# Kernel tuning notes

Measured on AMD Instinct MI355X. Metric: run time of the kernel, lower is better.

Reference implementation:

```python
import jax, jax.numpy as jnp
import numpy as np

DIM = 1024
NUM_HEADS = 16
HEAD_DIM = DIM // NUM_HEADS
SCALE = HEAD_DIM ** -0.5


def setup_inputs() -> dict:
    key = jax.random.key(0)
    k_x, k_qkv, k_proj, k_pb = jax.random.split(key, 4)
    B, N = 4, 2048
    x = jax.random.normal(k_x, (B, N, DIM), dtype=jnp.float32)
    # qkv: Linear(dim, 3*dim), qkv_bias=False -> no bias
    W_qkv = jax.random.normal(k_qkv, (DIM, 3 * DIM), dtype=jnp.float32) * (DIM ** -0.5)
    # proj: Linear(dim, dim) with bias (nn.Linear default)
    W_proj = jax.random.normal(k_proj, (DIM, DIM), dtype=jnp.float32) * (DIM ** -0.5)
    b_proj = jax.random.normal(k_pb, (DIM,), dtype=jnp.float32) * 0.01
    return {"x": x, "W_qkv": W_qkv, "W_proj": W_proj, "b_proj": b_proj}


def reference(x, W_qkv, W_proj, b_proj):
    B, N, C = x.shape
    H, D = NUM_HEADS, HEAD_DIM
    # qkv projection -> [B, N, 3, H, D] -> q,k,v each [B, H, N, D]
    qkv = (x @ W_qkv).reshape(B, N, 3, H, D)
    q, k, v = (jnp.moveaxis(qkv, 2, 0).transpose(0, 1, 3, 2, 4))  # [3,B,H,N,D]
    # attention scores [B, H, N, N], scaled QK^T (full matrix, as in source)
    attn = jnp.einsum('bhqd,bhkd->bhqk', q, k) * SCALE
    attn = jax.nn.softmax(attn, axis=-1)
    # attn @ V -> [B, H, N, D] -> [B, N, C]
    out = jnp.einsum('bhqk,bhkd->bhqd', attn, v)
    out = out.transpose(0, 2, 1, 3).reshape(B, N, C)
    # output projection
    return out @ W_proj + b_proj
```

## Files before the change

kernel.cpp:

```cpp
#include <hip/hip_runtime.h>
#include <hip/hip_bf16.h>

typedef __attribute__((ext_vector_type(8))) short short8;
typedef __attribute__((ext_vector_type(4))) short short4_t;
typedef __attribute__((ext_vector_type(4))) float floatx4;
typedef unsigned short u16;
typedef unsigned int u32;

#define SEQ 2048
#define NH 16
#define HD 64
#define CDIM 1024
#define MTOT 8192

__device__ __forceinline__ u16 f2bf(float f) {
  u32 u = __builtin_bit_cast(u32, f);
  u32 r = u + 0x7FFFu + ((u >> 16) & 1u);
  return (u16)(r >> 16);
}

__device__ __forceinline__ void gload16(const void* g, void* l) {
  __builtin_amdgcn_global_load_lds(
      (const __attribute__((address_space(1))) u32*)g,
      (__attribute__((address_space(3))) u32*)l, 16, 0, 0);
}

__global__ void cvt_x_kernel(const float* __restrict__ x, u16* __restrict__ xb) {
  size_t i = (size_t)blockIdx.x * 256 + threadIdx.x;
  const float4* xv = (const float4*)x;
  float4 a = xv[2 * i], c = xv[2 * i + 1];
  union { u16 h[8]; short8 v; } u;
  u.h[0] = f2bf(a.x); u.h[1] = f2bf(a.y); u.h[2] = f2bf(a.z); u.h[3] = f2bf(a.w);
  u.h[4] = f2bf(c.x); u.h[5] = f2bf(c.y); u.h[6] = f2bf(c.z); u.h[7] = f2bf(c.w);
  *(short8*)(xb + 8 * i) = u.v;
}

__global__ void transpose_w(const float* __restrict__ w, u16* __restrict__ wt,
                            int K, int N) {
  __shared__ float t[32][33];
  int n0 = blockIdx.x * 32, k0 = blockIdx.y * 32;
  int tr = threadIdx.x >> 5, tc = threadIdx.x & 31;
#pragma unroll
  for (int i = 0; i < 4; i++) {
    int r = tr + i * 8;
    t[r][tc] = w[(size_t)(k0 + r) * N + n0 + tc];
  }
  __syncthreads();
#pragma unroll
  for (int i = 0; i < 4; i++) {
    int r = tr + i * 8;
    wt[(size_t)(n0 + r) * K + k0 + tc] = f2bf(t[tc][r]);
  }
}

__global__ __launch_bounds__(256, 2) void gemm_qkv(
    const u16* __restrict__ A, const u16* __restrict__ BT,
    u16* __restrict__ qb, u16* __restrict__ kb, u16* __restrict__ vtb) {
  __shared__ u16 Ab[128 * 64];
  __shared__ u16 Bb[128 * 64];
  const int tid = threadIdx.x;
  const int w = tid >> 6, l = tid & 63;
  const int quad = l >> 4, l15 = l & 15;
  const int m0 = blockIdx.x * 128, n0 = blockIdx.y * 128;
  const int wr = w >> 1, wc = w & 1;

  floatx4 acc[4][4] = {};

  for (int k0 = 0; k0 < 1024; k0 += 64) {
    __syncthreads();
#pragma unroll
    for (int rnd = 0; rnd < 4; rnd++) {
      int ci = rnd * 256 + tid;
      int r = ci >> 3, pos = ci & 7;
      int c = pos ^ (r & 7);
      gload16(A + (size_t)(m0 + r) * 1024 + k0 + c * 8, (char*)Ab + ci * 16);
      gload16(BT + (size_t)(n0 + r) * 1024 + k0 + c * 8, (char*)Bb + ci * 16);
    }
    __syncthreads();
    short8 af[4][2], bf[4][2];
#pragma unroll
    for (int t = 0; t < 4; t++) {
      int ra = wr * 64 + t * 16 + l15;
      int ga = ra & 7;
#pragma unroll
      for (int ks = 0; ks < 2; ks++)
        af[t][ks] = *(short8*)((char*)Ab + ra * 128 + ((ks * 4 + quad) ^ ga) * 16);
      int rb = wc * 64 + t * 16 + l15;
      int gb = rb & 7;
#pragma unroll
      for (int ks = 0; ks < 2; ks++)
        bf[t][ks] = *(short8*)((char*)Bb + rb * 128 + ((ks * 4 + quad) ^ gb) * 16);
    }
#pragma unroll
    for (int ks = 0; ks < 2; ks++)
#pragma unroll
      for (int i = 0; i < 4; i++)
#pragma unroll
        for (int j = 0; j < 4; j++)
          acc[i][j] = __builtin_amdgcn_mfma_f32_16x16x32_bf16(af[i][ks], bf[j][ks], acc[i][j], 0, 0, 0);
  }

#pragma unroll
  for (int i = 0; i < 4; i++)
#pragma unroll
    for (int j = 0; j < 4; j++)
#pragma unroll
      for (int r = 0; r < 4; r++) {
        int m = m0 + wr * 64 + i * 16 + quad * 4 + r;
        int c = n0 + wc * 64 + j * 16 + l15;
        int b = m >> 11, n = m & 2047;
        int t = c >> 10, rem = c & 1023;
        int h = rem >> 6, d = rem & 63;
        int bh = b * NH + h;
        if (t == 0)      qb[((size_t)bh * SEQ + n) * HD + d] = f2bf(acc[i][j][r] * 0.18033688011112042f);
        else if (t == 1) kb[((size_t)bh * SEQ + n) * HD + d] = f2bf(acc[i][j][r]);
        else             vtb[((size_t)bh * HD + d) * SEQ + n] = f2bf(acc[i][j][r]);
      }
}

__global__ __launch_bounds__(256, 2) void gemm_proj(
    const u16* __restrict__ A, const u16* __restrict__ BT,
    const float* __restrict__ bias, float* __restrict__ out) {
  __shared__ u16 Ab[128 * 64];
  __shared__ u16 Bb[128 * 64];
  const int tid = threadIdx.x;
  const int w = tid >> 6, l = tid & 63;
  const int quad = l >> 4, l15 = l & 15;
  const int m0 = blockIdx.x * 128, n0 = blockIdx.y * 128;
  const int wr = w >> 1, wc = w & 1;

  floatx4 acc[4][4] = {};

  for (int k0 = 0; k0 < 1024; k0 += 64) {
    __syncthreads();
#pragma unroll
    for (int rnd = 0; rnd < 4; rnd++) {
      int ci = rnd * 256 + tid;
      int r = ci >> 3, pos = ci & 7;
      int c = pos ^ (r & 7);
      gload16(A + (size_t)(m0 + r) * 1024 + k0 + c * 8, (char*)Ab + ci * 16);
      gload16(BT + (size_t)(n0 + r) * 1024 + k0 + c * 8, (char*)Bb + ci * 16);
    }
    __syncthreads();
    short8 af[4][2], bf[4][2];
#pragma unroll
    for (int t = 0; t < 4; t++) {
      int ra = wr * 64 + t * 16 + l15;
      int ga = ra & 7;
#pragma unroll
      for (int ks = 0; ks < 2; ks++)
        af[t][ks] = *(short8*)((char*)Ab + ra * 128 + ((ks * 4 + quad) ^ ga) * 16);
      int rb = wc * 64 + t * 16 + l15;
      int gb = rb & 7;
#pragma unroll
      for (int ks = 0; ks < 2; ks++)
        bf[t][ks] = *(short8*)((char*)Bb + rb * 128 + ((ks * 4 + quad) ^ gb) * 16);
    }
#pragma unroll
    for (int ks = 0; ks < 2; ks++)
#pragma unroll
      for (int i = 0; i < 4; i++)
#pragma unroll
        for (int j = 0; j < 4; j++)
          acc[i][j] = __builtin_amdgcn_mfma_f32_16x16x32_bf16(af[i][ks], bf[j][ks], acc[i][j], 0, 0, 0);
  }

#pragma unroll
  for (int i = 0; i < 4; i++)
#pragma unroll
    for (int j = 0; j < 4; j++)
#pragma unroll
      for (int r = 0; r < 4; r++) {
        int m = m0 + wr * 64 + i * 16 + quad * 4 + r;
        int c = n0 + wc * 64 + j * 16 + l15;
        out[(size_t)m * CDIM + c] = acc[i][j][r] + bias[c];
      }
}

__global__ __launch_bounds__(256, 2) void attn_kernel(
    const u16* __restrict__ Qb, const u16* __restrict__ Kb,
    const u16* __restrict__ Vtb, u16* __restrict__ attnb) {
  __shared__ char smem[65536];
  const int tid = threadIdx.x;
  const int w = tid >> 6, l = tid & 63;
  const int quad = l >> 4, l15 = l & 15;

  const int lb = blockIdx.x + (blockIdx.y << 3);
  const int bh = ((lb & 7) << 3) + ((lb >> 3) & 7);
  const int qt0 = (lb >> 6) * 256;

  const u16* Kbase = Kb + (size_t)bh * SEQ * HD;
  const u16* Vbase = Vtb + (size_t)bh * HD * SEQ;

  short8 qf[4][2];
#pragma unroll
  for (int rt = 0; rt < 4; rt++) {
    int qrow = qt0 + w * 64 + rt * 16 + l15;
#pragma unroll
    for (int ks = 0; ks < 2; ks++)
      qf[rt][ks] = *(const short8*)(Qb + ((size_t)bh * SEQ + qrow) * HD + ks * 32 + quad * 8);
  }

  floatx4 O[4][4] = {};
  floatx4 sumacc[4] = {};

  union { u16 h[8]; short8 v; } onesu;
#pragma unroll
  for (int z = 0; z < 8; z++) onesu.h[z] = 0x3F80;
  const short8 ones = onesu.v;

  auto stage = [&](int n0, char* base) {
#pragma unroll
    for (int rnd = 0; rnd < 4; rnd++) {
      int ci = rnd * 256 + tid;
      int r = ci >> 3, pos = ci & 7;
      int c = pos ^ ((r & 7) ^ ((r >> 1) & 4));
      gload16(Kbase + (size_t)(n0 + r) * HD + c * 8, base + ci * 16);
    }
#pragma unroll
    for (int rnd = 0; rnd < 4; rnd++) {
      int ci = rnd * 256 + tid;
      int r = ci >> 4, pos = ci & 15;
      int c = pos ^ (r & 15);
      gload16(Vbase + (size_t)r * SEQ + n0 + c * 8, base + 16384 + ci * 16);
    }
  };

  stage(0, smem);
  __syncthreads();

  for (int kt = 0; kt < 16; kt++) {
    char* cur = smem + (kt & 1) * 32768;
    if (kt < 15) stage((kt + 1) * 128, smem + ((kt + 1) & 1) * 32768);

    char* KtC = cur;
    char* VtsC = cur + 16384;
#pragma unroll
    for (int p = 0; p < 4; p++) {
      floatx4 s[2][4];
#pragma unroll
      for (int t = 0; t < 2; t++) {
        int rho = p * 32 + (l15 >> 2) * 8 + t * 4 + (l15 & 3);
        int g = (rho & 7) ^ ((rho >> 1) & 4);
        short8 kf0 = *(short8*)(KtC + rho * 128 + ((0 + quad) ^ g) * 16);
        short8 kf1 = *(short8*)(KtC + rho * 128 + ((4 + quad) ^ g) * 16);
#pragma unroll
        for (int rt = 0; rt < 4; rt++) {
          floatx4 z = {};
          z = __builtin_amdgcn_mfma_f32_16x16x32_bf16(kf0, qf[rt][0], z, 0, 0, 0);
          z = __builtin_amdgcn_mfma_f32_16x16x32_bf16(kf1, qf[rt][1], z, 0, 0, 0);
          s[t][rt] = z;
        }
      }
      short8 pf[4];
#pragma unroll
      for (int rt = 0; rt < 4; rt++) {
        union { u32 d[4]; short8 v; } pu;
#pragma unroll
        for (int t = 0; t < 2; t++) {
          float e0 = __builtin_amdgcn_exp2f(s[t][rt][0]);
          float e1 = __builtin_amdgcn_exp2f(s[t][rt][1]);
          float e2 = __builtin_amdgcn_exp2f(s[t][rt][2]);
          float e3 = __builtin_amdgcn_exp2f(s[t][rt][3]);
          pu.d[t * 2 + 0] = __builtin_amdgcn_perm(
              __builtin_bit_cast(u32, e1), __builtin_bit_cast(u32, e0), 0x07060302u);
          pu.d[t * 2 + 1] = __builtin_amdgcn_perm(
              __builtin_bit_cast(u32, e3), __builtin_bit_cast(u32, e2), 0x07060302u);
        }
        pf[rt] = pu.v;
        sumacc[rt] = __builtin_amdgcn_mfma_f32_16x16x32_bf16(ones, pf[rt], sumacc[rt], 0, 0, 0);
      }
#pragma unroll
      for (int dt = 0; dt < 4; dt++) {
        int rv = dt * 16 + l15;
        short8 vf = *(short8*)(VtsC + rv * 256 + ((p * 4 + quad) ^ (rv & 15)) * 16);
#pragma unroll
        for (int rt = 0; rt < 4; rt++)
          O[rt][dt] = __builtin_amdgcn_mfma_f32_16x16x32_bf16(vf, pf[rt], O[rt][dt], 0, 0, 0);
      }
    }
    __syncthreads();
  }

  float inv[4];
#pragma unroll
  for (int rt = 0; rt < 4; rt++) inv[rt] = 1.f / sumacc[rt][0];

#pragma unroll
  for (int rt = 0; rt < 4; rt++)
#pragma unroll
    for (int dt = 0; dt < 4; dt++) {
      union { u16 h[4]; short4_t v; } pk;
#pragma unroll
      for (int r = 0; r < 4; r++) pk.h[r] = f2bf(O[rt][dt][r] * inv[rt]);
      *(short4_t*)(smem + (w * 64 + rt * 16 + l15) * 144 + (dt * 16 + quad * 4) * 2) = pk.v;
    }
  __syncthreads();
  {
    const int b = bh >> 4, h = bh & 15;
#pragma unroll
    for (int it = 0; it < 2; it++) {
      int row = it * 128 + (tid >> 1);
      int half = tid & 1;
      u16* gp = attnb + ((size_t)(b * SEQ + qt0 + row)) * CDIM + h * 64 + half * 32;
      char* lp = smem + row * 144 + half * 64;
#pragma unroll
      for (int c = 0; c < 4; c++)
        *(short8*)(gp + c * 8) = *(short8*)(lp + c * 16);
    }
  }
}

extern "C" void kernel_launch(void* const* d_in, const int* in_sizes, int n_in,
                              void* d_out, int out_size, void* d_ws, size_t ws_size,
                              hipStream_t stream) {
  const float* x = (const float*)d_in[0];
  const float* Wqkv = (const float*)d_in[1];
  const float* Wproj = (const float*)d_in[2];
  const float* bproj = (const float*)d_in[3];
  float* out = (float*)d_out;

  u16* xb = (u16*)d_ws;
  u16* wqkvT = xb + (size_t)8388608;
  u16* wprojT = wqkvT + (size_t)3145728;
  u16* qb = wprojT + (size_t)1048576;
  u16* kb = qb + (size_t)8388608;
  u16* vtb = kb + (size_t)8388608;
  u16* attnb = xb;

  cvt_x_kernel<<<4096, 256, 0, stream>>>(x, xb);
  transpose_w<<<dim3(96, 32), 256, 0, stream>>>(Wqkv, wqkvT, 1024, 3072);
  transpose_w<<<dim3(32, 32), 256, 0, stream>>>(Wproj, wprojT, 1024, 1024);
  gemm_qkv<<<dim3(64, 24), 256, 0, stream>>>(xb, wqkvT, qb, kb, vtb);
  attn_kernel<<<dim3(8, 64), 256, 0, stream>>>(qb, kb, vtb, attnb);
  gemm_proj<<<dim3(64, 8), 256, 0, stream>>>(attnb, wprojT, bproj, out);
}
```

Measured before the change: 242.4 us.

## Fuse x bf16 conversion into QKV GEMM and merge weight transposes into one launch

Drops the separate x-to-bf16 conversion kernel. The QKV GEMM now loads fp32 x tiles straight into LDS with a 16-chunk swizzle and packs them to bf16 (truncating) in registers before the MFMAs. The two weight-transpose launches are merged into a single prep kernel. This removes one full pass over x and two launches, but doubles the A-tile LDS footprint and global traffic per k-step, which may reduce occupancy. It also changes the rounding of x from round-to-nearest to truncation.

```diff
diff --git a/kernel.cpp b/kernel.cpp
--- a/kernel.cpp
+++ b/kernel.cpp
@@ -25,20 +25,20 @@
       (__attribute__((address_space(3))) u32*)l, 16, 0, 0);
 }
 
-__global__ void cvt_x_kernel(const float* __restrict__ x, u16* __restrict__ xb) {
-  size_t i = (size_t)blockIdx.x * 256 + threadIdx.x;
-  const float4* xv = (const float4*)x;
-  float4 a = xv[2 * i], c = xv[2 * i + 1];
-  union { u16 h[8]; short8 v; } u;
-  u.h[0] = f2bf(a.x); u.h[1] = f2bf(a.y); u.h[2] = f2bf(a.z); u.h[3] = f2bf(a.w);
-  u.h[4] = f2bf(c.x); u.h[5] = f2bf(c.y); u.h[6] = f2bf(c.z); u.h[7] = f2bf(c.w);
-  *(short8*)(xb + 8 * i) = u.v;
-}
-
-__global__ void transpose_w(const float* __restrict__ w, u16* __restrict__ wt,
-                            int K, int N) {
+__device__ __forceinline__ u32 pack2(float a, float b) {
+  return __builtin_amdgcn_perm(__builtin_bit_cast(u32, b),
+                               __builtin_bit_cast(u32, a), 0x07060302u);
+}
+
+__global__ void prep_kernel(const float* __restrict__ Wqkv, u16* __restrict__ wqkvT,
+                            const float* __restrict__ Wproj, u16* __restrict__ wprojT) {
   __shared__ float t[32][33];
-  int n0 = blockIdx.x * 32, k0 = blockIdx.y * 32;
+  int bid = blockIdx.x;
+  const float* w; u16* wt; int N, nb, kb;
+  if (bid < 3072) { w = Wqkv; wt = wqkvT; N = 3072; nb = bid % 96; kb = bid / 96; }
+  else { int tt = bid - 3072; w = Wproj; wt = wprojT; N = 1024; nb = tt % 32; kb = tt / 32; }
+  const int K = 1024;
+  int n0 = nb * 32, k0 = kb * 32;
   int tr = threadIdx.x >> 5, tc = threadIdx.x & 31;
 #pragma unroll
   for (int i = 0; i < 4; i++) {
@@ -54,9 +54,9 @@
 }
 
 __global__ __launch_bounds__(256, 2) void gemm_qkv(
-    const u16* __restrict__ A, const u16* __restrict__ BT,
+    const float* __restrict__ X, const u16* __restrict__ BT,
     u16* __restrict__ qb, u16* __restrict__ kb, u16* __restrict__ vtb) {
-  __shared__ u16 Ab[128 * 64];
+  __shared__ float Af[128 * 64];
   __shared__ u16 Bb[128 * 64];
   const int tid = threadIdx.x;
   const int w = tid >> 6, l = tid & 63;
@@ -69,11 +69,17 @@
   for (int k0 = 0; k0 < 1024; k0 += 64) {
     __syncthreads();
 #pragma unroll
+    for (int rnd = 0; rnd < 8; rnd++) {
+      int ci = rnd * 256 + tid;
+      int r = ci >> 4, pos = ci & 15;
+      int c = pos ^ (r & 15);
+      gload16(X + (size_t)(m0 + r) * 1024 + k0 + c * 4, (char*)Af + ci * 16);
+    }
+#pragma unroll
     for (int rnd = 0; rnd < 4; rnd++) {
       int ci = rnd * 256 + tid;
       int r = ci >> 3, pos = ci & 7;
       int c = pos ^ (r & 7);
-      gload16(A + (size_t)(m0 + r) * 1024 + k0 + c * 8, (char*)Ab + ci * 16);
       gload16(BT + (size_t)(n0 + r) * 1024 + k0 + c * 8, (char*)Bb + ci * 16);
     }
     __syncthreads();
@@ -81,10 +87,19 @@
 #pragma unroll
     for (int t = 0; t < 4; t++) {
       int ra = wr * 64 + t * 16 + l15;
-      int ga = ra & 7;
-#pragma unroll
-      for (int ks = 0; ks < 2; ks++)
-        af[t][ks] = *(short8*)((char*)Ab + ra * 128 + ((ks * 4 + quad) ^ ga) * 16);
+      int ga = ra & 15;
+#pragma unroll
+      for (int ks = 0; ks < 2; ks++) {
+        int cc = 2 * (ks * 4 + quad);
+        float4 lo = *(float4*)((char*)Af + ra * 256 + ((cc)     ^ ga) * 16);
+        float4 hi = *(float4*)((char*)Af + ra * 256 + ((cc + 1) ^ ga) * 16);
+        union { u32 d[4]; short8 v; } pk;
+        pk.d[0] = pack2(lo.x, lo.y);
+        pk.d[1] = pack2(lo.z, lo.w);
+        pk.d[2] = pack2(hi.x, hi.y);
+        pk.d[3] = pack2(hi.z, hi.w);
+        af[t][ks] = pk.v;
+      }
       int rb = wc * 64 + t * 16 + l15;
       int gb = rb & 7;
 #pragma unroll
@@ -320,18 +335,15 @@
   const float* bproj = (const float*)d_in[3];
   float* out = (float*)d_out;
 
-  u16* xb = (u16*)d_ws;
-  u16* wqkvT = xb + (size_t)8388608;
+  u16* wqkvT = (u16*)d_ws;
   u16* wprojT = wqkvT + (size_t)3145728;
   u16* qb = wprojT + (size_t)1048576;
   u16* kb = qb + (size_t)8388608;
   u16* vtb = kb + (size_t)8388608;
-  u16* attnb = xb;
-
-  cvt_x_kernel<<<4096, 256, 0, stream>>>(x, xb);
-  transpose_w<<<dim3(96, 32), 256, 0, stream>>>(Wqkv, wqkvT, 1024, 3072);
-  transpose_w<<<dim3(32, 32), 256, 0, stream>>>(Wproj, wprojT, 1024, 1024);
-  gemm_qkv<<<dim3(64, 24), 256, 0, stream>>>(xb, wqkvT, qb, kb, vtb);
+  u16* attnb = vtb + (size_t)8388608;
+
+  prep_kernel<<<4096, 256, 0, stream>>>(Wqkv, wqkvT, Wproj, wprojT);
+  gemm_qkv<<<dim3(64, 24), 256, 0, stream>>>(x, wqkvT, qb, kb, vtb);
   attn_kernel<<<dim3(8, 64), 256, 0, stream>>>(qb, kb, vtb, attnb);
   gemm_proj<<<dim3(64, 8), 256, 0, stream>>>(attnb, wprojT, bproj, out);
 }
```

Measured after the change: 264.4 us. 9.1% more time.
